# Kernel tuning notes

Measured on AMD Instinct MI355X. Metric: run time of the kernel, lower is better.

## Reference

```python
import jax, jax.numpy as jnp
import numpy as np

D_MODEL = 256
NHEAD = 4
HEAD_DIM = D_MODEL // NHEAD
EPS = 1e-5


def layernorm(x, g, b):
    mu = jnp.mean(x, axis=-1, keepdims=True)
    var = jnp.mean((x - mu) ** 2, axis=-1, keepdims=True)
    return (x - mu) * jax.lax.rsqrt(var + EPS) * g + b


def setup_inputs() -> dict:
    key = jax.random.key(0)
    ks = jax.random.split(key, 16)
    bs, L, S = 2, 2048, 2048
    inp = {
        "x": jax.random.normal(ks[0], (bs, L, D_MODEL), jnp.float32),
        "source": jax.random.normal(ks[1], (bs, S, D_MODEL), jnp.float32),
        "x_pe": jax.random.normal(ks[2], (bs, L, D_MODEL), jnp.float32),
        "source_pe": jax.random.normal(ks[3], (bs, S, D_MODEL), jnp.float32),
        "x_mask": jax.random.randint(ks[4], (bs, L), 0, 2).astype(bool),
        "source_mask": jax.random.randint(ks[5], (bs, S), 0, 2).astype(bool),
        "compatibility": jax.random.uniform(ks[6], (bs, L, S), jnp.float32),
        # learned params (bias-free linears, two layernorms)
        "Wq": jax.random.normal(ks[7], (D_MODEL, D_MODEL), jnp.float32) * 0.05,
        "Wk": jax.random.normal(ks[8], (D_MODEL, D_MODEL), jnp.float32) * 0.05,
        "Wv": jax.random.normal(ks[9], (D_MODEL, D_MODEL), jnp.float32) * 0.05,
        "Wmerge": jax.random.normal(ks[10], (D_MODEL, D_MODEL), jnp.float32) * 0.05,
        "Wmlp1": jax.random.normal(ks[11], (2 * D_MODEL, 2 * D_MODEL), jnp.float32) * 0.05,
        "Wmlp2": jax.random.normal(ks[12], (2 * D_MODEL, D_MODEL), jnp.float32) * 0.05,
        "ln1_g": jnp.ones((D_MODEL,), jnp.float32),
        "ln1_b": jnp.zeros((D_MODEL,), jnp.float32),
        "ln2_g": jnp.ones((D_MODEL,), jnp.float32),
        "ln2_b": jnp.zeros((D_MODEL,), jnp.float32),
    }
    return inp


def reference(x, source, x_pe, source_pe, x_mask, source_mask, compatibility,
              Wq, Wk, Wv, Wmerge, Wmlp1, Wmlp2, ln1_g, ln1_b, ln2_g, ln2_b):
    bs = x.shape[0]
    # pe_type == 'sinusoidal': add PE before projections
    q_in = x + x_pe
    k_in = source + source_pe
    qw = (q_in @ Wq).reshape(bs, -1, NHEAD, HEAD_DIM)
    kw = (k_in @ Wk).reshape(bs, -1, NHEAD, HEAD_DIM)
    vw = (source @ Wv).reshape(bs, -1, NHEAD, HEAD_DIM)
    # scores (n, l, s, h)
    a = jnp.einsum('nlhd,nshd->nlsh', qw, kw)
    a = a * compatibility[..., None]
    mask = x_mask[:, :, None, None] & (~source_mask)[:, None, :, None]
    a = jnp.where(mask, -jnp.inf, a)
    a = a / jnp.sqrt(jnp.asarray(HEAD_DIM, a.dtype))
    a = jax.nn.softmax(a, axis=2)
    o = jnp.einsum('nlsh,nshd->nlhd', a, vw).reshape(bs, -1, D_MODEL)
    message = layernorm(o @ Wmerge, ln1_g, ln1_b)
    h = jnp.concatenate([x, message], axis=2)
    message = jax.nn.relu(h @ Wmlp1) @ Wmlp2
    message = layernorm(message, ln2_g, ln2_b)
    return x + message
```

## Files before the change

kernel.cpp:

```cpp
#include <hip/hip_runtime.h>
#include <cstddef>
#include <math.h>

#define D_MODEL 256
#define NHEAD 4
#define HEAD_DIM 64
#define BSZ 2
#define SEQ 2048
#define MROWS (BSZ * SEQ)

typedef __attribute__((ext_vector_type(8))) short short8;
typedef __attribute__((ext_vector_type(4))) float f32x4;

__device__ __forceinline__ ushort f2bf_bits(float f) {
    union { float f; unsigned u; } c; c.f = f;
    unsigned u = c.u + 0x7fffu + ((c.u >> 16) & 1u);
    return (ushort)(u >> 16);
}
__device__ __forceinline__ unsigned pk2(float lo, float hi) {
    return (unsigned)f2bf_bits(lo) | ((unsigned)f2bf_bits(hi) << 16);
}
__device__ __forceinline__ void store_bf8(ushort* p, float4 a, float4 b) {
    uint4 u = make_uint4(pk2(a.x, a.y), pk2(a.z, a.w), pk2(b.x, b.y), pk2(b.z, b.w));
    *(uint4*)p = u;
}

__global__ __launch_bounds__(256) void prep_k(
    const float* __restrict__ x, const float* __restrict__ xpe,
    const float* __restrict__ src, const float* __restrict__ spe,
    const float* __restrict__ Wq, const float* __restrict__ Wk,
    const float* __restrict__ Wv, const float* __restrict__ Wm,
    const float* __restrict__ W1, const float* __restrict__ W2,
    ushort* __restrict__ Qin, ushort* __restrict__ Kin,
    ushort* __restrict__ Sb, ushort* __restrict__ Xb,
    ushort* __restrict__ Wqt, ushort* __restrict__ Wkt,
    ushort* __restrict__ Wvt, ushort* __restrict__ Wmt,
    ushort* __restrict__ W1t, ushort* __restrict__ W2t)
{
    const int gb = blockIdx.x;
    if (gb < 512) {
        const int e0 = (gb * 256 + threadIdx.x) * 8;
        const float4 a0 = *(const float4*)&x[e0],   a1 = *(const float4*)&x[e0 + 4];
        const float4 p0 = *(const float4*)&xpe[e0], p1 = *(const float4*)&xpe[e0 + 4];
        const float4 s0 = *(const float4*)&src[e0], s1 = *(const float4*)&src[e0 + 4];
        const float4 q0 = *(const float4*)&spe[e0], q1 = *(const float4*)&spe[e0 + 4];
        store_bf8(&Xb[e0], a0, a1);
        store_bf8(&Qin[e0],
                  make_float4(a0.x + p0.x, a0.y + p0.y, a0.z + p0.z, a0.w + p0.w),
                  make_float4(a1.x + p1.x, a1.y + p1.y, a1.z + p1.z, a1.w + p1.w));
        store_bf8(&Sb[e0], s0, s1);
        store_bf8(&Kin[e0],
                  make_float4(s0.x + q0.x, s0.y + q0.y, s0.z + q0.z, s0.w + q0.w),
                  make_float4(s1.x + q1.x, s1.y + q1.y, s1.z + q1.z, s1.w + q1.w));
    } else {
        const int f0 = ((gb - 512) * 256 + threadIdx.x) * 16;
        const float* in; ushort* out; int Nd, ksh, r;
        if (f0 < 262144) {
            const int w = f0 >> 16; r = f0 & 65535; Nd = 256; ksh = 8;
            in  = (w == 0) ? Wq  : (w == 1) ? Wk  : (w == 2) ? Wv  : Wm;
            out = (w == 0) ? Wqt : (w == 1) ? Wkt : (w == 2) ? Wvt : Wmt;
        } else if (f0 < 524288) { r = f0 - 262144; Nd = 512; ksh = 9; in = W1; out = W1t; }
        else                    { r = f0 - 524288; Nd = 256; ksh = 9; in = W2; out = W2t; }
        const int n = r >> ksh, k = r & ((1 << ksh) - 1);
        ushort tmp[16];
#pragma unroll
        for (int i = 0; i < 16; i++) tmp[i] = f2bf_bits(in[(size_t)(k + i) * Nd + n]);
        *(uint4*)&out[r]     = *(uint4*)&tmp[0];
        *(uint4*)&out[r + 8] = *(uint4*)&tmp[8];
    }
}

template <int AMODE, bool RELU, int OMODE>
__global__ __launch_bounds__(256) void bgemm_k(
    const ushort* __restrict__ A1, const ushort* __restrict__ A2,
    const ushort* __restrict__ Bt, void* __restrict__ Cout,
    int Kdim, int Ndim)
{
    __shared__ __attribute__((aligned(16))) ushort As[64][72];
    __shared__ __attribute__((aligned(16))) ushort Bs[64][72];

    const int t = threadIdx.x, w = t >> 6, lane = t & 63;
    const int quad = lane >> 4, l16 = lane & 15;
    const int m0 = blockIdx.y * 64, n0 = blockIdx.x * 64;
    const int rS = t >> 2, kS = (t & 3) * 16;

    f32x4 acc[4] = {};

    for (int k0 = 0; k0 < Kdim; k0 += 64) {
        const ushort* pa;
        if (AMODE == 2) {
            pa = (k0 < 256) ? &A1[(size_t)(m0 + rS) * 256 + k0 + kS]
                            : &A2[(size_t)(m0 + rS) * 256 + (k0 - 256) + kS];
        } else {
            pa = &A1[(size_t)(m0 + rS) * Kdim + k0 + kS];
        }
        const uint4 va0 = *(const uint4*)pa, va1 = *(const uint4*)(pa + 8);
        const ushort* pb = &Bt[(size_t)(n0 + rS) * Kdim + k0 + kS];
        const uint4 vb0 = *(const uint4*)pb, vb1 = *(const uint4*)(pb + 8);

        __syncthreads();
        *(uint4*)&As[rS][kS] = va0; *(uint4*)&As[rS][kS + 8] = va1;
        *(uint4*)&Bs[rS][kS] = vb0; *(uint4*)&Bs[rS][kS + 8] = vb1;
        __syncthreads();

#pragma unroll
        for (int kc = 0; kc < 64; kc += 32) {
            const short8 aq = *(const short8*)&As[w * 16 + l16][kc + quad * 8];
#pragma unroll
            for (int ct = 0; ct < 4; ct++) {
                const short8 bk = *(const short8*)&Bs[ct * 16 + l16][kc + quad * 8];
                acc[ct] = __builtin_amdgcn_mfma_f32_16x16x32_bf16(aq, bk, acc[ct], 0, 0, 0);
            }
        }
    }

#pragma unroll
    for (int ct = 0; ct < 4; ct++) {
#pragma unroll
        for (int reg = 0; reg < 4; reg++) {
            const int grow = m0 + w * 16 + quad * 4 + reg;
            const int col  = n0 + ct * 16 + l16;
            float v = acc[ct][reg];
            if (RELU) v = fmaxf(v, 0.f);
            if (OMODE == 0) {
                ((float*)Cout)[(size_t)grow * Ndim + col] = v;
            } else if (OMODE == 1) {
                ((ushort*)Cout)[(size_t)grow * Ndim + col] = f2bf_bits(v);
            } else {
                const int b = grow >> 11, s = grow & 2047;
                ((ushort*)Cout)[((size_t)(b * 256 + col)) * 2048 + s] = f2bf_bits(v);
            }
        }
    }
}

__global__ __launch_bounds__(256, 4) void attn_k(
    const ushort* __restrict__ Q, const ushort* __restrict__ K,
    const ushort* __restrict__ Vt, const float* __restrict__ comp,
    const int* __restrict__ xmask, const int* __restrict__ smask,
    ushort* __restrict__ O)
{
    __shared__ __attribute__((aligned(16))) ushort Qs[64][72];
    __shared__ __attribute__((aligned(16))) ushort Ks[64][72];
    __shared__ __attribute__((aligned(16))) ushort Vs[64][72];
    __shared__ __attribute__((aligned(16))) ushort Ps[64][72];
    __shared__ int xms[64];
    __shared__ int sms[64];

    const int t    = threadIdx.x;
    const int w    = t >> 6;
    const int lane = t & 63;
    const int quad = lane >> 4;
    const int l16  = lane & 15;
    const int l0   = blockIdx.x * 64;
    const int h    = blockIdx.y, b = blockIdx.z;

#pragma unroll
    for (int i = 0; i < 2; i++) {
        const int e = t + i * 256, r = e >> 3, cg = (e & 7) * 8;
        *(uint4*)&Qs[r][cg] =
            *(const uint4*)&Q[((size_t)(b * SEQ + l0 + r)) * D_MODEL + h * HEAD_DIM + cg];
    }
    if (t < 64) xms[t] = xmask[b * SEQ + l0 + t];

    const int rowbase = w * 16 + quad * 4;
    const int arow    = w * 16 + l16;
    const float* crow = comp + ((size_t)b * SEQ + l0 + rowbase) * SEQ;

    float m_i[4] = {-INFINITY, -INFINITY, -INFINITY, -INFINITY};
    float l_i[4] = {0.f, 0.f, 0.f, 0.f};
    f32x4 oacc[4] = {};

    for (int s0 = 0; s0 < SEQ; s0 += 64) {
        __syncthreads();
#pragma unroll
        for (int i = 0; i < 2; i++) {
            const int e = t + i * 256, r = e >> 3, cg = (e & 7) * 8;
            *(uint4*)&Ks[r][cg] =
                *(const uint4*)&K[((size_t)(b * SEQ + s0 + r)) * D_MODEL + h * HEAD_DIM + cg];
            *(uint4*)&Vs[r][cg] =
                *(const uint4*)&Vt[((size_t)(b * 256 + h * HEAD_DIM + r)) * SEQ + s0 + cg];
        }
        if (t < 64) sms[t] = smask[b * SEQ + s0 + t];

        float cv[16];
#pragma unroll
        for (int reg = 0; reg < 4; reg++)
#pragma unroll
            for (int ct = 0; ct < 4; ct++)
                cv[reg * 4 + ct] = crow[(size_t)reg * SEQ + s0 + ct * 16 + l16];

        __syncthreads();

        f32x4 sacc[4] = {};
#pragma unroll
        for (int kc = 0; kc < 64; kc += 32) {
            const short8 aq = *(const short8*)&Qs[arow][kc + quad * 8];
#pragma unroll
            for (int ct = 0; ct < 4; ct++) {
                const short8 bk = *(const short8*)&Ks[ct * 16 + l16][kc + quad * 8];
                sacc[ct] = __builtin_amdgcn_mfma_f32_16x16x32_bf16(aq, bk, sacc[ct], 0, 0, 0);
            }
        }

        const int sm0 = sms[l16], sm1 = sms[16 + l16], sm2 = sms[32 + l16], sm3 = sms[48 + l16];
        float sc[4][4];
        float rm[4];
#pragma unroll
        for (int reg = 0; reg < 4; reg++) {
            const bool xm = (xms[rowbase + reg] != 0);
            float s0v = sacc[0][reg] * cv[reg * 4 + 0] * 0.125f;
            float s1v = sacc[1][reg] * cv[reg * 4 + 1] * 0.125f;
            float s2v = sacc[2][reg] * cv[reg * 4 + 2] * 0.125f;
            float s3v = sacc[3][reg] * cv[reg * 4 + 3] * 0.125f;
            if (xm) {
                if (sm0 == 0) s0v = -1e30f;
                if (sm1 == 0) s1v = -1e30f;
                if (sm2 == 0) s2v = -1e30f;
                if (sm3 == 0) s3v = -1e30f;
            }
            sc[0][reg] = s0v; sc[1][reg] = s1v; sc[2][reg] = s2v; sc[3][reg] = s3v;
            rm[reg] = fmaxf(fmaxf(s0v, s1v), fmaxf(s2v, s3v));
        }
#pragma unroll
        for (int off = 1; off < 16; off <<= 1)
#pragma unroll
            for (int reg = 0; reg < 4; reg++)
                rm[reg] = fmaxf(rm[reg], __shfl_xor(rm[reg], off, 64));

        float alpha[4], psum[4];
#pragma unroll
        for (int reg = 0; reg < 4; reg++) {
            const float m_new = fmaxf(m_i[reg], rm[reg]);
            alpha[reg] = __expf(m_i[reg] - m_new);
            m_i[reg] = m_new;
            float ps = 0.f;
#pragma unroll
            for (int ct = 0; ct < 4; ct++) {
                const float p = __expf(sc[ct][reg] - m_new);
                ps += p;
                Ps[rowbase + reg][ct * 16 + l16] = f2bf_bits(p);
            }
            psum[reg] = ps;
        }
#pragma unroll
        for (int off = 1; off < 16; off <<= 1)
#pragma unroll
            for (int reg = 0; reg < 4; reg++)
                psum[reg] += __shfl_xor(psum[reg], off, 64);
#pragma unroll
        for (int reg = 0; reg < 4; reg++)
            l_i[reg] = l_i[reg] * alpha[reg] + psum[reg];
#pragma unroll
        for (int ct = 0; ct < 4; ct++)
#pragma unroll
            for (int reg = 0; reg < 4; reg++) oacc[ct][reg] *= alpha[reg];

#pragma unroll
        for (int kc = 0; kc < 64; kc += 32) {
            const short8 ap = *(const short8*)&Ps[arow][kc + quad * 8];
#pragma unroll
            for (int ct = 0; ct < 4; ct++) {
                const short8 bv = *(const short8*)&Vs[ct * 16 + l16][kc + quad * 8];
                oacc[ct] = __builtin_amdgcn_mfma_f32_16x16x32_bf16(ap, bv, oacc[ct], 0, 0, 0);
            }
        }
    }

    float inv[4];
#pragma unroll
    for (int reg = 0; reg < 4; reg++) inv[reg] = 1.f / l_i[reg];
#pragma unroll
    for (int ct = 0; ct < 4; ct++)
#pragma unroll
        for (int reg = 0; reg < 4; reg++) {
            const int grow = b * SEQ + l0 + rowbase + reg;
            O[(size_t)grow * D_MODEL + h * HEAD_DIM + ct * 16 + l16] =
                f2bf_bits(oacc[ct][reg] * inv[reg]);
        }
}

template <bool RESID, bool BF16OUT>
__global__ __launch_bounds__(256) void ln_k(
    const float* __restrict__ in, const float* __restrict__ g,
    const float* __restrict__ bta, const float* __restrict__ resid,
    void* __restrict__ out)
{
    const int row = blockIdx.x, t = threadIdx.x;
    const float v = in[(size_t)row * 256 + t];
    float s = v, s2 = v * v;
#pragma unroll
    for (int off = 1; off < 64; off <<= 1) {
        s  += __shfl_xor(s, off, 64);
        s2 += __shfl_xor(s2, off, 64);
    }
    __shared__ float red[2][4];
    const int w = t >> 6, ln = t & 63;
    if (ln == 0) { red[0][w] = s; red[1][w] = s2; }
    __syncthreads();
    s  = red[0][0] + red[0][1] + red[0][2] + red[0][3];
    s2 = red[1][0] + red[1][1] + red[1][2] + red[1][3];
    const float mu  = s * (1.f / 256.f);
    const float var = s2 * (1.f / 256.f) - mu * mu;
    const float r   = rsqrtf(var + 1e-5f);
    float o = (v - mu) * r * g[t] + bta[t];
    if (RESID) o += resid[(size_t)row * 256 + t];
    if (BF16OUT) ((ushort*)out)[(size_t)row * 256 + t] = f2bf_bits(o);
    else         ((float*)out)[(size_t)row * 256 + t] = o;
}

extern "C" void kernel_launch(void* const* d_in, const int* in_sizes, int n_in,
                              void* d_out, int out_size, void* d_ws, size_t ws_size,
                              hipStream_t stream)
{
    (void)in_sizes; (void)n_in; (void)out_size; (void)ws_size;
    const float* x      = (const float*)d_in[0];
    const float* source = (const float*)d_in[1];
    const float* x_pe   = (const float*)d_in[2];
    const float* s_pe   = (const float*)d_in[3];
    const int*   x_mask = (const int*)d_in[4];
    const int*   s_mask = (const int*)d_in[5];
    const float* comp   = (const float*)d_in[6];
    const float* Wq     = (const float*)d_in[7];
    const float* Wk     = (const float*)d_in[8];
    const float* Wv     = (const float*)d_in[9];
    const float* Wmerge = (const float*)d_in[10];
    const float* Wmlp1  = (const float*)d_in[11];
    const float* Wmlp2  = (const float*)d_in[12];
    const float* ln1_g  = (const float*)d_in[13];
    const float* ln1_b  = (const float*)d_in[14];
    const float* ln2_g  = (const float*)d_in[15];
    const float* ln2_b  = (const float*)d_in[16];
    float* out = (float*)d_out;
    char*  ws  = (char*)d_ws;

    const size_t MB = 1024 * 1024;
    ushort* Qin   = (ushort*)(ws + 0 * MB);
    ushort* Kin   = (ushort*)(ws + 2 * MB);
    ushort* Sb    = (ushort*)(ws + 4 * MB);
    ushort* Xb    = (ushort*)(ws + 6 * MB);
    ushort* Qb    = (ushort*)(ws + 8 * MB);
    ushort* Kb    = (ushort*)(ws + 10 * MB);
    ushort* VtG   = (ushort*)(ws + 12 * MB);
    ushort* Obf   = (ushort*)(ws + 0 * MB);
    float*  Mg    = (float*)(ws + 2 * MB);
    ushort* Msg1b = (ushort*)(ws + 8 * MB);
    ushort* H     = (ushort*)(ws + 10 * MB);
    float*  M2    = (float*)(ws + 14 * MB);
    ushort* Wqt   = (ushort*)(ws + 18 * MB);
    ushort* Wkt   = (ushort*)(ws + 18 * MB + 128 * 1024);
    ushort* Wvt   = (ushort*)(ws + 18 * MB + 256 * 1024);
    ushort* Wmt   = (ushort*)(ws + 18 * MB + 384 * 1024);
    ushort* W1t   = (ushort*)(ws + 18 * MB + 512 * 1024);
    ushort* W2t   = (ushort*)(ws + 19 * MB);

    const dim3 g256(4, 64), g512(8, 64);

    prep_k<<<672, 256, 0, stream>>>(x, x_pe, source, s_pe,
        Wq, Wk, Wv, Wmerge, Wmlp1, Wmlp2,
        Qin, Kin, Sb, Xb, Wqt, Wkt, Wvt, Wmt, W1t, W2t);

    bgemm_k<0, false, 1><<<g256, 256, 0, stream>>>(Qin, nullptr, Wqt, Qb, 256, 256);
    bgemm_k<0, false, 1><<<g256, 256, 0, stream>>>(Kin, nullptr, Wkt, Kb, 256, 256);
    bgemm_k<0, false, 2><<<g256, 256, 0, stream>>>(Sb, nullptr, Wvt, VtG, 256, 256);

    attn_k<<<dim3(SEQ / 64, NHEAD, BSZ), 256, 0, stream>>>(
        Qb, Kb, VtG, comp, x_mask, s_mask, Obf);

    bgemm_k<0, false, 0><<<g256, 256, 0, stream>>>(Obf, nullptr, Wmt, Mg, 256, 256);
    ln_k<false, true><<<MROWS, 256, 0, stream>>>(Mg, ln1_g, ln1_b, nullptr, Msg1b);
    bgemm_k<2, true, 1><<<g512, 256, 0, stream>>>(Xb, Msg1b, W1t, H, 512, 512);
    bgemm_k<0, false, 0><<<g256, 256, 0, stream>>>(H, nullptr, W2t, M2, 512, 256);
    ln_k<true, false><<<MROWS, 256, 0, stream>>>(M2, ln2_g, ln2_b, x, out);
}
```

Before: 232.2 us.

## Split attention over source chunks, fuse QKV GEMMs, drop LDS staging in GEMM

```diff
diff --git a/kernel.cpp b/kernel.cpp
--- a/kernel.cpp
+++ b/kernel.cpp
@@ -8,6 +8,8 @@
 #define BSZ 2
 #define SEQ 2048
 #define MROWS (BSZ * SEQ)
+#define NSPLIT 4
+#define SCHUNK (SEQ / NSPLIT)
 
 typedef __attribute__((ext_vector_type(8))) short short8;
 typedef __attribute__((ext_vector_type(4))) float f32x4;
@@ -16,6 +18,10 @@
     union { float f; unsigned u; } c; c.f = f;
     unsigned u = c.u + 0x7fffu + ((c.u >> 16) & 1u);
     return (ushort)(u >> 16);
+}
+__device__ __forceinline__ float bf2f(ushort u) {
+    union { unsigned u; float f; } c; c.u = (unsigned)u << 16;
+    return c.f;
 }
 __device__ __forceinline__ unsigned pk2(float lo, float hi) {
     return (unsigned)f2bf_bits(lo) | ((unsigned)f2bf_bits(hi) << 16);
@@ -70,47 +76,33 @@
     }
 }
 
-template <int AMODE, bool RELU, int OMODE>
+template <int AMODE, bool RELU, int OMODE, int KD, int ND>
 __global__ __launch_bounds__(256) void bgemm_k(
     const ushort* __restrict__ A1, const ushort* __restrict__ A2,
-    const ushort* __restrict__ Bt, void* __restrict__ Cout,
-    int Kdim, int Ndim)
-{
-    __shared__ __attribute__((aligned(16))) ushort As[64][72];
-    __shared__ __attribute__((aligned(16))) ushort Bs[64][72];
-
+    const ushort* __restrict__ Bt, void* __restrict__ Cout)
+{
     const int t = threadIdx.x, w = t >> 6, lane = t & 63;
     const int quad = lane >> 4, l16 = lane & 15;
     const int m0 = blockIdx.y * 64, n0 = blockIdx.x * 64;
-    const int rS = t >> 2, kS = (t & 3) * 16;
+    const int arow = m0 + w * 16 + l16;
 
     f32x4 acc[4] = {};
 
-    for (int k0 = 0; k0 < Kdim; k0 += 64) {
+#pragma unroll
+    for (int k0 = 0; k0 < KD; k0 += 32) {
         const ushort* pa;
         if (AMODE == 2) {
-            pa = (k0 < 256) ? &A1[(size_t)(m0 + rS) * 256 + k0 + kS]
-                            : &A2[(size_t)(m0 + rS) * 256 + (k0 - 256) + kS];
+            pa = (k0 < 256) ? &A1[(size_t)arow * 256 + k0 + quad * 8]
+                            : &A2[(size_t)arow * 256 + (k0 - 256) + quad * 8];
         } else {
-            pa = &A1[(size_t)(m0 + rS) * Kdim + k0 + kS];
-        }
-        const uint4 va0 = *(const uint4*)pa, va1 = *(const uint4*)(pa + 8);
-        const ushort* pb = &Bt[(size_t)(n0 + rS) * Kdim + k0 + kS];
-        const uint4 vb0 = *(const uint4*)pb, vb1 = *(const uint4*)(pb + 8);
-
-        __syncthreads();
-        *(uint4*)&As[rS][kS] = va0; *(uint4*)&As[rS][kS + 8] = va1;
-        *(uint4*)&Bs[rS][kS] = vb0; *(uint4*)&Bs[rS][kS + 8] = vb1;
-        __syncthreads();
-
-#pragma unroll
-        for (int kc = 0; kc < 64; kc += 32) {
-            const short8 aq = *(const short8*)&As[w * 16 + l16][kc + quad * 8];
-#pragma unroll
-            for (int ct = 0; ct < 4; ct++) {
-                const short8 bk = *(const short8*)&Bs[ct * 16 + l16][kc + quad * 8];
-                acc[ct] = __builtin_amdgcn_mfma_f32_16x16x32_bf16(aq, bk, acc[ct], 0, 0, 0);
-            }
+            pa = &A1[(size_t)arow * KD + k0 + quad * 8];
+        }
+        const short8 aq = *(const short8*)pa;
+#pragma unroll
+        for (int ct = 0; ct < 4; ct++) {
+            const short8 bk =
+                *(const short8*)&Bt[(size_t)(n0 + ct * 16 + l16) * KD + k0 + quad * 8];
+            acc[ct] = __builtin_amdgcn_mfma_f32_16x16x32_bf16(aq, bk, acc[ct], 0, 0, 0);
         }
     }
 
@@ -122,13 +114,53 @@
             const int col  = n0 + ct * 16 + l16;
             float v = acc[ct][reg];
             if (RELU) v = fmaxf(v, 0.f);
-            if (OMODE == 0) {
-                ((float*)Cout)[(size_t)grow * Ndim + col] = v;
-            } else if (OMODE == 1) {
-                ((ushort*)Cout)[(size_t)grow * Ndim + col] = f2bf_bits(v);
+            if (OMODE == 0) ((float*)Cout)[(size_t)grow * ND + col] = v;
+            else            ((ushort*)Cout)[(size_t)grow * ND + col] = f2bf_bits(v);
+        }
+    }
+}
+
+__global__ __launch_bounds__(256) void qkv_k(
+    const ushort* __restrict__ Qin, const ushort* __restrict__ Kin,
+    const ushort* __restrict__ Sb,
+    const ushort* __restrict__ Wqt, const ushort* __restrict__ Wkt,
+    const ushort* __restrict__ Wvt,
+    ushort* __restrict__ Qb, ushort* __restrict__ Kb, ushort* __restrict__ VtG)
+{
+    const int z = blockIdx.z;
+    const ushort* A  = (z == 0) ? Qin : (z == 1) ? Kin : Sb;
+    const ushort* Bt = (z == 0) ? Wqt : (z == 1) ? Wkt : Wvt;
+    ushort* out      = (z == 0) ? Qb  : (z == 1) ? Kb  : VtG;
+
+    const int t = threadIdx.x, w = t >> 6, lane = t & 63;
+    const int quad = lane >> 4, l16 = lane & 15;
+    const int m0 = blockIdx.y * 64, n0 = blockIdx.x * 64;
+    const int arow = m0 + w * 16 + l16;
+
+    f32x4 acc[4] = {};
+#pragma unroll
+    for (int k0 = 0; k0 < 256; k0 += 32) {
+        const short8 aq = *(const short8*)&A[(size_t)arow * 256 + k0 + quad * 8];
+#pragma unroll
+        for (int ct = 0; ct < 4; ct++) {
+            const short8 bk =
+                *(const short8*)&Bt[(size_t)(n0 + ct * 16 + l16) * 256 + k0 + quad * 8];
+            acc[ct] = __builtin_amdgcn_mfma_f32_16x16x32_bf16(aq, bk, acc[ct], 0, 0, 0);
+        }
+    }
+
+#pragma unroll
+    for (int ct = 0; ct < 4; ct++) {
+#pragma unroll
+        for (int reg = 0; reg < 4; reg++) {
+            const int grow = m0 + w * 16 + quad * 4 + reg;
+            const int col  = n0 + ct * 16 + l16;
+            const ushort v = f2bf_bits(acc[ct][reg]);
+            if (z < 2) {
+                out[(size_t)grow * 256 + col] = v;
             } else {
                 const int b = grow >> 11, s = grow & 2047;
-                ((ushort*)Cout)[((size_t)(b * 256 + col)) * 2048 + s] = f2bf_bits(v);
+                out[((size_t)(b * 256 + col)) * 2048 + s] = v;
             }
         }
     }
@@ -138,7 +170,7 @@
     const ushort* __restrict__ Q, const ushort* __restrict__ K,
     const ushort* __restrict__ Vt, const float* __restrict__ comp,
     const int* __restrict__ xmask, const int* __restrict__ smask,
-    ushort* __restrict__ O)
+    ushort* __restrict__ Opart, float2* __restrict__ ml)
 {
     __shared__ __attribute__((aligned(16))) ushort Qs[64][72];
     __shared__ __attribute__((aligned(16))) ushort Ks[64][72];
@@ -153,7 +185,10 @@
     const int quad = lane >> 4;
     const int l16  = lane & 15;
     const int l0   = blockIdx.x * 64;
-    const int h    = blockIdx.y, b = blockIdx.z;
+    const int h    = blockIdx.y;
+    const int b    = blockIdx.z >> 2;
+    const int sc   = blockIdx.z & 3;
+    const int sbeg = sc * SCHUNK;
 
 #pragma unroll
     for (int i = 0; i < 2; i++) {
@@ -171,7 +206,7 @@
     float l_i[4] = {0.f, 0.f, 0.f, 0.f};
     f32x4 oacc[4] = {};
 
-    for (int s0 = 0; s0 < SEQ; s0 += 64) {
+    for (int s0 = sbeg; s0 < sbeg + SCHUNK; s0 += 64) {
         __syncthreads();
 #pragma unroll
         for (int i = 0; i < 2; i++) {
@@ -204,7 +239,7 @@
         }
 
         const int sm0 = sms[l16], sm1 = sms[16 + l16], sm2 = sms[32 + l16], sm3 = sms[48 + l16];
-        float sc[4][4];
+        float scv[4][4];
         float rm[4];
 #pragma unroll
         for (int reg = 0; reg < 4; reg++) {
@@ -219,7 +254,7 @@
                 if (sm2 == 0) s2v = -1e30f;
                 if (sm3 == 0) s3v = -1e30f;
             }
-            sc[0][reg] = s0v; sc[1][reg] = s1v; sc[2][reg] = s2v; sc[3][reg] = s3v;
+            scv[0][reg] = s0v; scv[1][reg] = s1v; scv[2][reg] = s2v; scv[3][reg] = s3v;
             rm[reg] = fmaxf(fmaxf(s0v, s1v), fmaxf(s2v, s3v));
         }
 #pragma unroll
@@ -237,7 +272,7 @@
             float ps = 0.f;
 #pragma unroll
             for (int ct = 0; ct < 4; ct++) {
-                const float p = __expf(sc[ct][reg] - m_new);
+                const float p = (scv[ct][reg] >= -1e29f) ? __expf(scv[ct][reg] - m_new) : 0.f;
                 ps += p;
                 Ps[rowbase + reg][ct * 16 + l16] = f2bf_bits(p);
             }
@@ -267,17 +302,44 @@
         }
     }
 
-    float inv[4];
-#pragma unroll
-    for (int reg = 0; reg < 4; reg++) inv[reg] = 1.f / l_i[reg];
 #pragma unroll
     for (int ct = 0; ct < 4; ct++)
 #pragma unroll
         for (int reg = 0; reg < 4; reg++) {
             const int grow = b * SEQ + l0 + rowbase + reg;
-            O[(size_t)grow * D_MODEL + h * HEAD_DIM + ct * 16 + l16] =
-                f2bf_bits(oacc[ct][reg] * inv[reg]);
-        }
+            Opart[((size_t)sc * MROWS + grow) * D_MODEL + h * HEAD_DIM + ct * 16 + l16] =
+                f2bf_bits(oacc[ct][reg]);
+        }
+    if (l16 == 0) {
+#pragma unroll
+        for (int reg = 0; reg < 4; reg++) {
+            const int grow = b * SEQ + l0 + rowbase + reg;
+            ml[((size_t)sc * MROWS + grow) * NHEAD + h] = make_float2(m_i[reg], l_i[reg]);
+        }
+    }
+}
+
+__global__ __launch_bounds__(256) void amerge_k(
+    const ushort* __restrict__ Opart, const float2* __restrict__ ml,
+    ushort* __restrict__ Obf)
+{
+    const int row = blockIdx.x, t = threadIdx.x, h = t >> 6;
+    float mm[NSPLIT], llv[NSPLIT];
+    float M = -INFINITY;
+#pragma unroll
+    for (int c = 0; c < NSPLIT; c++) {
+        const float2 v = ml[((size_t)c * MROWS + row) * NHEAD + h];
+        mm[c] = v.x; llv[c] = v.y;
+        M = fmaxf(M, v.x);
+    }
+    float num = 0.f, den = 0.f;
+#pragma unroll
+    for (int c = 0; c < NSPLIT; c++) {
+        const float e = __expf(mm[c] - M);
+        den += llv[c] * e;
+        num += bf2f(Opart[((size_t)c * MROWS + row) * D_MODEL + t]) * e;
+    }
+    Obf[(size_t)row * D_MODEL + t] = f2bf_bits(num / den);
 }
 
 template <bool RESID, bool BF16OUT>
@@ -336,40 +398,40 @@
 
     const size_t MB = 1024 * 1024;
     ushort* Qin   = (ushort*)(ws + 0 * MB);
+    float2* ml    = (float2*)(ws + 0 * MB);
     ushort* Kin   = (ushort*)(ws + 2 * MB);
+    ushort* Obf   = (ushort*)(ws + 2 * MB);
     ushort* Sb    = (ushort*)(ws + 4 * MB);
     ushort* Xb    = (ushort*)(ws + 6 * MB);
     ushort* Qb    = (ushort*)(ws + 8 * MB);
+    ushort* Msg1b = (ushort*)(ws + 8 * MB);
     ushort* Kb    = (ushort*)(ws + 10 * MB);
+    ushort* H     = (ushort*)(ws + 10 * MB);
     ushort* VtG   = (ushort*)(ws + 12 * MB);
-    ushort* Obf   = (ushort*)(ws + 0 * MB);
-    float*  Mg    = (float*)(ws + 2 * MB);
-    ushort* Msg1b = (ushort*)(ws + 8 * MB);
-    ushort* H     = (ushort*)(ws + 10 * MB);
-    float*  M2    = (float*)(ws + 14 * MB);
-    ushort* Wqt   = (ushort*)(ws + 18 * MB);
-    ushort* Wkt   = (ushort*)(ws + 18 * MB + 128 * 1024);
-    ushort* Wvt   = (ushort*)(ws + 18 * MB + 256 * 1024);
-    ushort* Wmt   = (ushort*)(ws + 18 * MB + 384 * 1024);
-    ushort* W1t   = (ushort*)(ws + 18 * MB + 512 * 1024);
-    ushort* W2t   = (ushort*)(ws + 19 * MB);
-
-    const dim3 g256(4, 64), g512(8, 64);
+    ushort* Opart = (ushort*)(ws + 14 * MB);
+    float*  Mg    = (float*)(ws + 14 * MB);
+    float*  M2    = (float*)(ws + 18 * MB);
+    ushort* Wqt   = (ushort*)(ws + 22 * MB);
+    ushort* Wkt   = (ushort*)(ws + 22 * MB + 128 * 1024);
+    ushort* Wvt   = (ushort*)(ws + 22 * MB + 256 * 1024);
+    ushort* Wmt   = (ushort*)(ws + 22 * MB + 384 * 1024);
+    ushort* W1t   = (ushort*)(ws + 22 * MB + 512 * 1024);
+    ushort* W2t   = (ushort*)(ws + 23 * MB);
 
     prep_k<<<672, 256, 0, stream>>>(x, x_pe, source, s_pe,
         Wq, Wk, Wv, Wmerge, Wmlp1, Wmlp2,
         Qin, Kin, Sb, Xb, Wqt, Wkt, Wvt, Wmt, W1t, W2t);
 
-    bgemm_k<0, false, 1><<<g256, 256, 0, stream>>>(Qin, nullptr, Wqt, Qb, 256, 256);
-    bgemm_k<0, false, 1><<<g256, 256, 0, stream>>>(Kin, nullptr, Wkt, Kb, 256, 256);
-    bgemm_k<0, false, 2><<<g256, 256, 0, stream>>>(Sb, nullptr, Wvt, VtG, 256, 256);
-
-    attn_k<<<dim3(SEQ / 64, NHEAD, BSZ), 256, 0, stream>>>(
-        Qb, Kb, VtG, comp, x_mask, s_mask, Obf);
-
-    bgemm_k<0, false, 0><<<g256, 256, 0, stream>>>(Obf, nullptr, Wmt, Mg, 256, 256);
+    qkv_k<<<dim3(4, 64, 3), 256, 0, stream>>>(Qin, Kin, Sb, Wqt, Wkt, Wvt, Qb, Kb, VtG);
+
+    attn_k<<<dim3(SEQ / 64, NHEAD, BSZ * NSPLIT), 256, 0, stream>>>(
+        Qb, Kb, VtG, comp, x_mask, s_mask, Opart, ml);
+
+    amerge_k<<<MROWS, 256, 0, stream>>>(Opart, ml, Obf);
+
+    bgemm_k<0, false, 0, 256, 256><<<dim3(4, 64), 256, 0, stream>>>(Obf, nullptr, Wmt, Mg);
     ln_k<false, true><<<MROWS, 256, 0, stream>>>(Mg, ln1_g, ln1_b, nullptr, Msg1b);
-    bgemm_k<2, true, 1><<<g512, 256, 0, stream>>>(Xb, Msg1b, W1t, H, 512, 512);
-    bgemm_k<0, false, 0><<<g256, 256, 0, stream>>>(H, nullptr, W2t, M2, 512, 256);
+    bgemm_k<2, true, 1, 512, 512><<<dim3(8, 64), 256, 0, stream>>>(Xb, Msg1b, W1t, H);
+    bgemm_k<0, false, 0, 512, 256><<<dim3(4, 64), 256, 0, stream>>>(H, nullptr, W2t, M2);
     ln_k<true, false><<<MROWS, 256, 0, stream>>>(M2, ln2_g, ln2_b, x, out);
 }
```

Result: faster. 220.7 us (-5.0%).
